# Optimization experiments

Measured on AMD Instinct MI355X. Metric: run time of the kernel, lower is better.

## Reference

```python
import math
import jax, jax.numpy as jnp
import numpy as np

B, T, DIN, DH, E, TOPK = 2048, 512, 32, 96, 6, 2


def setup_inputs() -> dict:
    key = jax.random.key(0)
    ks = jax.random.split(key, 20)
    x = jax.random.normal(ks[0], (B, T, DIN), jnp.float32)
    lengths = jax.random.randint(ks[1], (B,), 1, T + 1)
    mask = (jnp.arange(T)[None, :] < lengths[:, None])

    def U(k, shape, fan):
        s = 1.0 / math.sqrt(fan)
        return jax.random.uniform(k, shape, jnp.float32, -s, s)

    # PyTorch LSTM init: U(-1/sqrt(DH), 1/sqrt(DH)); gate order i,f,g,o
    Wih = U(ks[2], (4 * DH, DIN), DH)
    Whh = U(ks[3], (4 * DH, DH), DH)
    bih = U(ks[4], (4 * DH,), DH)
    bhh = U(ks[5], (4 * DH,), DH)
    Wq = U(ks[6], (DH, DH), DH); bq = U(ks[7], (DH,), DH)
    Wk = U(ks[8], (DH, DH), DH); bk = U(ks[9], (DH,), DH)
    Wv = U(ks[10], (DH, DH), DH); bv = U(ks[11], (DH,), DH)
    Wg = U(ks[12], (E, 2 * DH), 2 * DH); bg = U(ks[13], (E,), 2 * DH)
    We1 = U(ks[14], (E, DH, 2 * DH), 2 * DH); be1 = U(ks[15], (E, DH), 2 * DH)
    We2 = U(ks[16], (E, DH), DH); be2 = U(ks[17], (E,), DH)
    return dict(x=x, lengths=lengths, mask=mask, Wih=Wih, Whh=Whh, bih=bih, bhh=bhh,
                Wq=Wq, bq=bq, Wk=Wk, bk=bk, Wv=Wv, bv=bv, Wg=Wg, bg=bg,
                We1=We1, be1=be1, We2=We2, be2=be2)


def _lstm(x, mask, Wih, Whh, bih, bhh):
    # packed-sequence semantics: carry frozen past each sample's length,
    # padded output positions zeroed (like pad_packed_sequence).
    xg = x @ Wih.T + bih  # [B,T,4*DH] precomputed input projection
    dh = Whh.shape[1]

    def step(carry, inp):
        h, c = carry
        xg_t, m_t = inp
        g = xg_t + h @ Whh.T + bhh
        i, f, gg, o = jnp.split(g, 4, axis=-1)
        c_new = jax.nn.sigmoid(f) * c + jax.nn.sigmoid(i) * jnp.tanh(gg)
        h_new = jax.nn.sigmoid(o) * jnp.tanh(c_new)
        m = m_t[:, None]
        h = jnp.where(m, h_new, h)
        c = jnp.where(m, c_new, c)
        return (h, c), jnp.where(m, h_new, 0.0)

    init = (jnp.zeros((x.shape[0], dh), x.dtype), jnp.zeros((x.shape[0], dh), x.dtype))
    (hT, _), H = jax.lax.scan(step, init, (jnp.swapaxes(xg, 0, 1), mask.T))
    return jnp.swapaxes(H, 0, 1), hT  # H:[B,T,DH], hT:[B,DH]


def reference(x, lengths, mask, Wih, Whh, bih, bhh, Wq, bq, Wk, bk, Wv, bv,
              Wg, bg, We1, be1, We2, be2):
    H, hT = _lstm(x, mask, Wih, Whh, bih, bhh)
    Q = hT @ Wq.T + bq                      # [B,DH]
    K = H @ Wk.T + bk                       # [B,T,DH]
    V = H @ Wv.T + bv                       # [B,T,DH]
    logits = jnp.einsum('bd,btd->bt', Q, K) / math.sqrt(K.shape[-1])
    logits = jnp.where(mask, logits, -1e9)
    alpha = jax.nn.softmax(logits, axis=1)  # [B,T]
    ctx = jnp.einsum('bt,btd->bd', alpha, V)
    feats = jnp.concatenate([ctx, hT], axis=-1)  # [B,2*DH]
    gate_logits = feats @ Wg.T + bg              # [B,E]
    topv, topi = jax.lax.top_k(gate_logits, TOPK)
    pi = jax.nn.softmax(topv, axis=-1)           # [B,TOPK]
    # all-expert dense compute (E tiny), then gather selected -> same math as
    # the per-expert masked scatter loop in the torch module (dropout off).
    h1 = jax.nn.relu(jnp.einsum('bf,ehf->beh', feats, We1) + be1[None])  # [B,E,DH]
    outs = jnp.einsum('beh,eh->be', h1, We2) + be2[None]                  # [B,E]
    sel = jnp.take_along_axis(outs, topi, axis=1)                         # [B,TOPK]
    yhat = jnp.sum(pi * sel, axis=-1, keepdims=True)                      # [B,1]
    return yhat, alpha, gate_logits
```

## Files before the change

### kernel.cpp

```cpp
#include <hip/hip_runtime.h>
#include <hip/hip_bf16.h>

#define B_ 2048
#define T_ 512
#define DIN_ 32
#define DH_ 96
#define NG_ 384
#define E_ 6

#define BPB 8
#define HP 104
#define GS 10

typedef __attribute__((ext_vector_type(8))) _Float16 f16x8;
typedef __attribute__((ext_vector_type(4))) float f32x4;

#if defined(__has_builtin)
# if __has_builtin(__builtin_amdgcn_exp2f)
#  define EXP2F(x) __builtin_amdgcn_exp2f(x)
# endif
# if __has_builtin(__builtin_amdgcn_rcpf)
#  define RCPF(x) __builtin_amdgcn_rcpf(x)
# endif
#endif
#ifndef EXP2F
# define EXP2F(x) exp2f(x)
#endif
#ifndef RCPF
# define RCPF(x) (1.0f/(x))
#endif

__device__ __forceinline__ float sigf(float x) {
    return RCPF(1.0f + EXP2F(x * -1.44269504f));
}
__device__ __forceinline__ float tanhf_(float x) {
    return 1.0f - 2.0f * RCPF(1.0f + EXP2F(x * 2.88539008f));
}

__device__ __forceinline__ f16x8 cvt8(float4 a, float4 b) {
    f16x8 r;
    r[0] = (_Float16)a.x; r[1] = (_Float16)a.y; r[2] = (_Float16)a.z; r[3] = (_Float16)a.w;
    r[4] = (_Float16)b.x; r[5] = (_Float16)b.y; r[6] = (_Float16)b.z; r[7] = (_Float16)b.w;
    return r;
}
__device__ __forceinline__ f16x8 cvt8p(const float* p) {
    return cvt8(*(const float4*)p, *(const float4*)(p + 4));
}

__device__ __forceinline__ void lds_barrier() {
    asm volatile("s_waitcnt lgkmcnt(0)\n\ts_barrier" ::: "memory");
}

__global__ __launch_bounds__(512) void sort_kernel(
    const int* __restrict__ lengths, int* __restrict__ perm) {
    __shared__ int sbins[512];
    __shared__ int soffs[512];
    const int tid = threadIdx.x;
    sbins[tid] = 0;
    __syncthreads();
    for (int b = tid; b < B_; b += 512) atomicAdd(&sbins[lengths[b] - 1], 1);
    __syncthreads();
    soffs[tid] = sbins[tid];
    __syncthreads();
    for (int d = 1; d < 512; d <<= 1) {
        int v = (tid >= d) ? soffs[tid - d] : 0;
        __syncthreads();
        soffs[tid] += v;
        __syncthreads();
    }
    int excl = soffs[tid] - sbins[tid];
    __syncthreads();
    soffs[tid] = excl;
    __syncthreads();
    for (int b = tid; b < B_; b += 512) {
        const int pos = atomicAdd(&soffs[lengths[b] - 1], 1);
        perm[pos] = b;
    }
}

__global__ __launch_bounds__(768, 1) void lstm_kernel(
    const float* __restrict__ x, const int* __restrict__ lengths,
    const int* __restrict__ perm,
    const float* __restrict__ Wih, const float* __restrict__ Whh,
    const float* __restrict__ bih, const float* __restrict__ bhh,
    _Float16* __restrict__ Hout, float* __restrict__ hT)
{
    __shared__ float sgate[NG_ * GS];
    __shared__ _Float16 sh[2][8 * HP];
    __shared__ int sgb[BPB], slen[BPB];

    const int tid  = threadIdx.x;
    const int bb   = blockIdx.x * BPB;
    const int wave = tid >> 6;
    const int lane = tid & 63;
    const int col  = lane & 15;
    const int quad = lane >> 4;

    if (tid < BPB) {
        const int g = perm[bb + tid];
        sgb[tid] = g;
        slen[tid] = lengths[g];
    }
    {
        _Float16* shf = &sh[0][0];
        for (int i = tid; i < 2 * 8 * HP; i += 768) shf[i] = (_Float16)0.f;
    }
    __syncthreads();

    int bmax = slen[0];
#pragma unroll
    for (int i = 1; i < BPB; ++i) bmax = max(bmax, slen[i]);

    int gc[2]; float bias[2];
    f16x8 wh[2][3], wi[2];
#pragma unroll
    for (int j = 0; j < 2; ++j) {
        const int tau = wave * 2 + j;
        const int g = tau / 6, u6 = tau % 6;
        const int gcj = g * DH_ + u6 * 16 + col;
        gc[j] = gcj;
#pragma unroll
        for (int kf = 0; kf < 3; ++kf)
            wh[j][kf] = cvt8p(Whh + gcj * DH_ + kf * 32 + quad * 8);
        wi[j] = cvt8p(Wih + gcj * DIN_ + quad * 8);
        bias[j] = bih[gcj] + bhh[gcj];
    }

    const int eu = tid >> 3;
    const int eb = tid & 7;
    float c1 = 0.f, hk1 = 0.f;
    const int len1 = slen[eb];

    const bool st_act = tid < 384;
    const int sb = tid / 48;
    const int su = (tid % 48) * 2;
    _Float16* Hst = Hout + ((long long)sgb[sb] * T_) * DH_ + su;

    const bool arow = col < 8;
    const float* xp = x + ((long long)sgb[col & 7] * T_) * DIN_ + quad * 8;
    float4 xc0 = make_float4(0.f, 0.f, 0.f, 0.f), xc1 = xc0;
    if (arow) { xc0 = *(const float4*)xp; xc1 = *(const float4*)(xp + 4); }

    for (int t = 0; t < bmax; ++t) {
        const int buf = t & 1;

        f16x8 h0 = 0, h1 = 0, h2 = 0;
        if (arow) {
            const _Float16* hrow = &sh[buf][col * HP];
            h0 = *(const f16x8*)(hrow + 0  + quad * 8);
            h1 = *(const f16x8*)(hrow + 32 + quad * 8);
            h2 = *(const f16x8*)(hrow + 64 + quad * 8);
        }

        const float* xpn = (t + 1 < T_) ? (xp + DIN_) : xp;
        float4 xn0 = make_float4(0.f, 0.f, 0.f, 0.f), xn1 = xn0;
        if (arow) { xn0 = *(const float4*)xpn; xn1 = *(const float4*)(xpn + 4); }

        f16x8 xa = cvt8(xc0, xc1);

#pragma unroll
        for (int j = 0; j < 2; ++j) {
            f32x4 a = {bias[j], bias[j], bias[j], bias[j]};
            a = __builtin_amdgcn_mfma_f32_16x16x32_f16(h0, wh[j][0], a, 0, 0, 0);
            a = __builtin_amdgcn_mfma_f32_16x16x32_f16(h1, wh[j][1], a, 0, 0, 0);
            a = __builtin_amdgcn_mfma_f32_16x16x32_f16(h2, wh[j][2], a, 0, 0, 0);
            a = __builtin_amdgcn_mfma_f32_16x16x32_f16(xa, wi[j],    a, 0, 0, 0);
            if (quad < 2) {
                float2* sp = (float2*)&sgate[gc[j] * GS + quad * 4];
                sp[0] = float2{a[0], a[1]};
                sp[1] = float2{a[2], a[3]};
            }
        }
        lds_barrier();

        if (t > 0 && st_act) {
            unsigned v = *(const unsigned*)&sh[buf][sb * HP + su];
            *(unsigned*)Hst = v;
            Hst += DH_;
        }

        {
            float iv = sgate[(0 * DH_ + eu) * GS + eb];
            float fv = sgate[(1 * DH_ + eu) * GS + eb];
            float gv = sgate[(2 * DH_ + eu) * GS + eb];
            float ov = sgate[(3 * DH_ + eu) * GS + eb];
            float cn = sigf(fv) * c1 + sigf(iv) * tanhf_(gv);
            float hn = sigf(ov) * tanhf_(cn);
            const bool m = t < len1;
            c1  = m ? cn : c1;
            hk1 = m ? hn : hk1;
            sh[buf ^ 1][eb * HP + eu] = (_Float16)hk1;
        }
        lds_barrier();

        xp = xpn; xc0 = xn0; xc1 = xn1;
    }

    if (st_act) {
        unsigned v = *(const unsigned*)&sh[bmax & 1][sb * HP + su];
        *(unsigned*)Hst = v;
    }

    hT[sgb[eb] * DH_ + eu] = hk1;
}

__global__ __launch_bounds__(256) void attn_moe_kernel(
    const _Float16* __restrict__ H, const float* __restrict__ hT,
    const int* __restrict__ lengths,
    const float* __restrict__ Wq, const float* __restrict__ bq,
    const float* __restrict__ Wk, const float* __restrict__ bk,
    const float* __restrict__ Wv, const float* __restrict__ bv,
    const float* __restrict__ Wg, const float* __restrict__ bg,
    const float* __restrict__ We1, const float* __restrict__ be1,
    const float* __restrict__ We2, const float* __restrict__ be2,
    float* __restrict__ yhat_out, float* __restrict__ alpha_out,
    float* __restrict__ gl_out)
{
    __shared__ float salpha[T_];
    __shared__ float shT[DH_];
    __shared__ float sQ[DH_];
    __shared__ float sqk[DH_];
    __shared__ float spart[DH_];
    __shared__ float sfeats[2 * DH_];
    __shared__ float sh1[2][DH_];
    __shared__ float sred[4], ssum[4];
    __shared__ float sgl[E_];
    __shared__ float spi[2];
    __shared__ float souts[2];
    __shared__ float sqb_s;
    __shared__ int stopi[2];

    const int b = blockIdx.x, tid = threadIdx.x;
    const int len = lengths[b];
    const float scale = 0.10206207262f;

    if (tid < DH_) shT[tid] = hT[b * DH_ + tid];
    __syncthreads();
    if (tid < DH_) {
        float acc = bq[tid];
        const float* wr = Wq + tid * DH_;
        for (int d = 0; d < DH_; d += 4) {
            float4 w4 = *(const float4*)(wr + d);
            acc += w4.x * shT[d] + w4.y * shT[d + 1] + w4.z * shT[d + 2] + w4.w * shT[d + 3];
        }
        sQ[tid] = acc;
    }
    __syncthreads();
    if (tid < DH_) {
        float acc = 0.f;
        for (int j = 0; j < DH_; ++j) acc += Wk[j * DH_ + tid] * sQ[j];
        sqk[tid] = acc * scale;
    }
    if (tid >= 192) {
        const int ln = tid - 192;
        float p = sQ[ln] * bk[ln];
        if (ln < DH_ - 64) p += sQ[ln + 64] * bk[ln + 64];
        for (int off = 32; off; off >>= 1) p += __shfl_xor(p, off);
        if (ln == 0) sqb_s = p * scale;
    }
    __syncthreads();
    const float qbv = sqb_s;

    float lg[2]; bool vd[2];
#pragma unroll
    for (int hh = 0; hh < 2; ++hh) {
        const int t = tid + hh * 256;
        vd[hh] = t < len;
        float l = qbv;
        if (vd[hh]) {
            const _Float16* hr = H + ((long long)b * T_ + t) * DH_;
#pragma unroll
            for (int u = 0; u < DH_; u += 8) {
                f16x8 hv = *(const f16x8*)(hr + u);
                float4 qa = *(const float4*)&sqk[u];
                float4 qc = *(const float4*)&sqk[u + 4];
                l += (float)hv[0] * qa.x + (float)hv[1] * qa.y
                   + (float)hv[2] * qa.z + (float)hv[3] * qa.w
                   + (float)hv[4] * qc.x + (float)hv[5] * qc.y
                   + (float)hv[6] * qc.z + (float)hv[7] * qc.w;
            }
        }
        lg[hh] = l;
    }

    float m = fmaxf(vd[0] ? lg[0] : -1e30f, vd[1] ? lg[1] : -1e30f);
    for (int off = 32; off; off >>= 1) m = fmaxf(m, __shfl_xor(m, off));
    if ((tid & 63) == 0) sred[tid >> 6] = m;
    __syncthreads();
    m = fmaxf(fmaxf(sred[0], sred[1]), fmaxf(sred[2], sred[3]));

    float e0 = vd[0] ? EXP2F((lg[0] - m) * 1.44269504f) : 0.f;
    float e1 = vd[1] ? EXP2F((lg[1] - m) * 1.44269504f) : 0.f;
    float s = e0 + e1;
    for (int off = 32; off; off >>= 1) s += __shfl_xor(s, off);
    if ((tid & 63) == 0) ssum[tid >> 6] = s;
    __syncthreads();
    s = (ssum[0] + ssum[1]) + (ssum[2] + ssum[3]);

    const float rinv = RCPF(s);
    const float a0 = e0 * rinv, a1 = e1 * rinv;
    salpha[tid] = a0;
    salpha[tid + 256] = a1;
    alpha_out[(long long)b * T_ + tid] = a0;
    alpha_out[(long long)b * T_ + tid + 256] = a1;
    __syncthreads();

    if (tid < 192) {
        const int ub = tid >> 4, tl = tid & 15;
        float acc[8] = {0.f, 0.f, 0.f, 0.f, 0.f, 0.f, 0.f, 0.f};
        const _Float16* hb = H + ((long long)b * T_) * DH_ + ub * 8;
#pragma unroll 4
        for (int k = 0; k < 32; ++k) {
            const int t = tl + (k << 4);
            if (t < len) {
                f16x8 hv = *(const f16x8*)(hb + t * DH_);
                const float a = salpha[t];
#pragma unroll
                for (int i = 0; i < 8; ++i) acc[i] += a * (float)hv[i];
            }
        }
#pragma unroll
        for (int i = 0; i < 8; ++i) {
            acc[i] += __shfl_xor(acc[i], 1);
            acc[i] += __shfl_xor(acc[i], 2);
            acc[i] += __shfl_xor(acc[i], 4);
            acc[i] += __shfl_xor(acc[i], 8);
        }
        if (tl == 0) {
#pragma unroll
            for (int i = 0; i < 8; ++i) spart[ub * 8 + i] = acc[i];
        }
    }
    __syncthreads();

    if (tid < DH_) {
        float acc = bv[tid];
        const float* wr = Wv + tid * DH_;
        for (int u = 0; u < DH_; u += 4) {
            float4 w4 = *(const float4*)(wr + u);
            acc += w4.x * spart[u] + w4.y * spart[u + 1] + w4.z * spart[u + 2] + w4.w * spart[u + 3];
        }
        sfeats[tid] = acc;
        sfeats[DH_ + tid] = shT[tid];
    }
    __syncthreads();

    if (tid < 192) {
        const int e6 = tid >> 5, cc = tid & 31;
        float p = 0.f;
        const float* wg = Wg + e6 * 2 * DH_;
#pragma unroll
        for (int j = 0; j < 6; ++j) p += wg[cc * 6 + j] * sfeats[cc * 6 + j];
        for (int off = 16; off; off >>= 1) p += __shfl_xor(p, off);
        if (cc == 0) {
            float g = p + bg[e6];
            sgl[e6] = g;
            gl_out[b * E_ + e6] = g;
        }
    }
    __syncthreads();

    if (tid == 0) {
        int i0 = 0; float v0 = sgl[0];
        for (int ee = 1; ee < E_; ++ee) if (sgl[ee] > v0) { v0 = sgl[ee]; i0 = ee; }
        int i1 = -1; float v1 = -1e30f;
        for (int ee = 0; ee < E_; ++ee) {
            if (ee == i0) continue;
            if (sgl[ee] > v1) { v1 = sgl[ee]; i1 = ee; }
        }
        float ex1 = EXP2F((v1 - v0) * 1.44269504f);
        float inv = RCPF(1.f + ex1);
        spi[0] = inv; spi[1] = ex1 * inv;
        stopi[0] = i0; stopi[1] = i1;
    }
    __syncthreads();

    if (tid < 192) {
        const int e2 = tid / DH_, u = tid - e2 * DH_;
        const int ex = stopi[e2];
        float acc = be1[ex * DH_ + u];
        const float* w = We1 + ((long long)ex * DH_ + u) * (2 * DH_);
        for (int f = 0; f < 2 * DH_; f += 4) {
            float4 w4 = *(const float4*)(w + f);
            acc += w4.x * sfeats[f] + w4.y * sfeats[f + 1] + w4.z * sfeats[f + 2] + w4.w * sfeats[f + 3];
        }
        sh1[e2][u] = fmaxf(acc, 0.f);
    }
    __syncthreads();

    if (tid < 128) {
        const int e2 = tid >> 6, ln = tid & 63;
        const int ex = stopi[e2];
        const float* w2 = We2 + ex * DH_;
        float p = sh1[e2][ln] * w2[ln];
        if (ln < DH_ - 64) p += sh1[e2][ln + 64] * w2[ln + 64];
        for (int off = 32; off; off >>= 1) p += __shfl_xor(p, off);
        if (ln == 0) souts[e2] = p + be2[ex];
    }
    __syncthreads();
    if (tid == 0)
        yhat_out[b] = spi[0] * souts[0] + spi[1] * souts[1];
}

extern "C" void kernel_launch(void* const* d_in, const int* in_sizes, int n_in,
                              void* d_out, int out_size, void* d_ws, size_t ws_size,
                              hipStream_t stream) {
    const float* x   = (const float*)d_in[0];
    const int* lengths = (const int*)d_in[1];
    const float* Wih = (const float*)d_in[3];
    const float* Whh = (const float*)d_in[4];
    const float* bih = (const float*)d_in[5];
    const float* bhh = (const float*)d_in[6];
    const float* Wq  = (const float*)d_in[7];
    const float* bq  = (const float*)d_in[8];
    const float* Wk  = (const float*)d_in[9];
    const float* bk  = (const float*)d_in[10];
    const float* Wv  = (const float*)d_in[11];
    const float* bv  = (const float*)d_in[12];
    const float* Wg  = (const float*)d_in[13];
    const float* bg  = (const float*)d_in[14];
    const float* We1 = (const float*)d_in[15];
    const float* be1 = (const float*)d_in[16];
    const float* We2 = (const float*)d_in[17];
    const float* be2 = (const float*)d_in[18];

    float* yhat  = (float*)d_out;
    float* alpha = yhat + B_;
    float* gl    = alpha + (size_t)B_ * T_;

    char* ws = (char*)d_ws;
    _Float16* Hws = (_Float16*)ws;
    float* hTws = (float*)(ws + (size_t)B_ * T_ * DH_ * 2);
    int* perm   = (int*)(hTws + (size_t)B_ * DH_);

    sort_kernel<<<dim3(1), dim3(512), 0, stream>>>(lengths, perm);

    lstm_kernel<<<dim3(B_ / BPB), dim3(768), 0, stream>>>(
        x, lengths, perm, Wih, Whh, bih, bhh, Hws, hTws);
    attn_moe_kernel<<<dim3(B_), dim3(256), 0, stream>>>(
        Hws, hTws, lengths, Wq, bq, Wk, bk, Wv, bv, Wg, bg,
        We1, be1, We2, be2, yhat, alpha, gl);
}
```

Before: 697.9 us.

## Interleave two 8-sample LSTM groups per block to overlap MFMA with gate math

Each LSTM block now processes 16 sorted samples as two groups of 8. Their steps are software-pipelined so that one group's gate MFMAs run alongside the other group's elementwise cell update and H store, with a double-buffered gate array. This halves the block count and is meant to hide the serial matmul→activation latency of the recurrence. In exchange each step does more work between barriers, and bmax is now taken over 16 samples, which adds padding steps.

```diff
diff --git a/kernel.cpp b/kernel.cpp
--- a/kernel.cpp
+++ b/kernel.cpp
@@ -8,9 +8,9 @@
 #define NG_ 384
 #define E_ 6
 
-#define BPB 8
+#define BPB 16
 #define HP 104
-#define GS 10
+#define GS 12
 
 typedef __attribute__((ext_vector_type(8))) _Float16 f16x8;
 typedef __attribute__((ext_vector_type(4))) float f32x4;
@@ -85,8 +85,8 @@
     const float* __restrict__ bih, const float* __restrict__ bhh,
     _Float16* __restrict__ Hout, float* __restrict__ hT)
 {
-    __shared__ float sgate[NG_ * GS];
-    __shared__ _Float16 sh[2][8 * HP];
+    __shared__ float sgate[2][NG_ * GS];
+    __shared__ _Float16 sh[BPB * HP];
     __shared__ int sgb[BPB], slen[BPB];
 
     const int tid  = threadIdx.x;
@@ -101,10 +101,7 @@
         sgb[tid] = g;
         slen[tid] = lengths[g];
     }
-    {
-        _Float16* shf = &sh[0][0];
-        for (int i = tid; i < 2 * 8 * HP; i += 768) shf[i] = (_Float16)0.f;
-    }
+    for (int i = tid; i < BPB * HP; i += 768) sh[i] = (_Float16)0.f;
     __syncthreads();
 
     int bmax = slen[0];
@@ -128,35 +125,40 @@
 
     const int eu = tid >> 3;
     const int eb = tid & 7;
-    float c1 = 0.f, hk1 = 0.f;
-    const int len1 = slen[eb];
-
-    const bool st_act = tid < 384;
-    const int sb = tid / 48;
-    const int su = (tid % 48) * 2;
-    _Float16* Hst = Hout + ((long long)sgb[sb] * T_) * DH_ + su;
+    float cA = 0.f, hkA = 0.f, cB = 0.f, hkB = 0.f;
+    const int lenA = slen[eb];
+    const int lenB = slen[8 + eb];
+
+    const bool stA = tid < 384;
+    const int sbA = (tid / 48) & 7;
+    const int suA = (tid % 48) * 2;
+    const int sbB = ((tid - 384) / 48) & 7;
+    const int suB = ((tid - 384) % 48) * 2;
+    _Float16* HstA = Hout + ((long long)sgb[sbA] * T_) * DH_ + suA;
+    _Float16* HstB = Hout + ((long long)sgb[8 + sbB] * T_) * DH_ + suB;
 
     const bool arow = col < 8;
-    const float* xp = x + ((long long)sgb[col & 7] * T_) * DIN_ + quad * 8;
-    float4 xc0 = make_float4(0.f, 0.f, 0.f, 0.f), xc1 = xc0;
-    if (arow) { xc0 = *(const float4*)xp; xc1 = *(const float4*)(xp + 4); }
+    const float* xpA = x + ((long long)sgb[col & 7] * T_) * DIN_ + quad * 8;
+    const float* xpB = x + ((long long)sgb[8 + (col & 7)] * T_) * DIN_ + quad * 8;
+    float4 z4 = make_float4(0.f, 0.f, 0.f, 0.f);
+    float4 xA0 = z4, xA1 = z4, xB0 = z4, xB1 = z4;
+    if (arow) {
+        xA0 = *(const float4*)xpA; xA1 = *(const float4*)(xpA + 4);
+        xB0 = *(const float4*)xpB; xB1 = *(const float4*)(xpB + 4);
+    }
 
     for (int t = 0; t < bmax; ++t) {
-        const int buf = t & 1;
-
         f16x8 h0 = 0, h1 = 0, h2 = 0;
         if (arow) {
-            const _Float16* hrow = &sh[buf][col * HP];
-            h0 = *(const f16x8*)(hrow + 0  + quad * 8);
-            h1 = *(const f16x8*)(hrow + 32 + quad * 8);
-            h2 = *(const f16x8*)(hrow + 64 + quad * 8);
-        }
-
-        const float* xpn = (t + 1 < T_) ? (xp + DIN_) : xp;
-        float4 xn0 = make_float4(0.f, 0.f, 0.f, 0.f), xn1 = xn0;
-        if (arow) { xn0 = *(const float4*)xpn; xn1 = *(const float4*)(xpn + 4); }
-
-        f16x8 xa = cvt8(xc0, xc1);
+            const _Float16* hr = &sh[col * HP];
+            h0 = *(const f16x8*)(hr + 0  + quad * 8);
+            h1 = *(const f16x8*)(hr + 32 + quad * 8);
+            h2 = *(const f16x8*)(hr + 64 + quad * 8);
+        }
+        const float* xpAn = (t + 1 < T_) ? (xpA + DIN_) : xpA;
+        float4 xAn0 = z4, xAn1 = z4;
+        if (arow) { xAn0 = *(const float4*)xpAn; xAn1 = *(const float4*)(xpAn + 4); }
+        f16x8 xa = cvt8(xA0, xA1);
 
 #pragma unroll
         for (int j = 0; j < 2; ++j) {
@@ -165,43 +167,99 @@
             a = __builtin_amdgcn_mfma_f32_16x16x32_f16(h1, wh[j][1], a, 0, 0, 0);
             a = __builtin_amdgcn_mfma_f32_16x16x32_f16(h2, wh[j][2], a, 0, 0, 0);
             a = __builtin_amdgcn_mfma_f32_16x16x32_f16(xa, wi[j],    a, 0, 0, 0);
-            if (quad < 2) {
-                float2* sp = (float2*)&sgate[gc[j] * GS + quad * 4];
-                sp[0] = float2{a[0], a[1]};
-                sp[1] = float2{a[2], a[3]};
-            }
+            if (quad < 2)
+                *(f32x4*)&sgate[0][gc[j] * GS + quad * 4] = a;
+        }
+
+        if (t > 0) {
+            float iv = sgate[1][(0 * DH_ + eu) * GS + eb];
+            float fv = sgate[1][(1 * DH_ + eu) * GS + eb];
+            float gv = sgate[1][(2 * DH_ + eu) * GS + eb];
+            float ov = sgate[1][(3 * DH_ + eu) * GS + eb];
+            float cn = sigf(fv) * cB + sigf(iv) * tanhf_(gv);
+            float hn = sigf(ov) * tanhf_(cn);
+            const bool m = (t - 1) < lenB;
+            cB  = m ? cn : cB;
+            hkB = m ? hn : hkB;
+            sh[(8 + eb) * HP + eu] = (_Float16)hkB;
+        }
+        if (t > 0 && stA) {
+            unsigned v = *(const unsigned*)&sh[sbA * HP + suA];
+            *(unsigned*)HstA = v;
+            HstA += DH_;
         }
         lds_barrier();
 
-        if (t > 0 && st_act) {
-            unsigned v = *(const unsigned*)&sh[buf][sb * HP + su];
-            *(unsigned*)Hst = v;
-            Hst += DH_;
+        f16x8 g0 = 0, g1 = 0, g2 = 0;
+        if (arow) {
+            const _Float16* hr = &sh[(8 + col) * HP];
+            g0 = *(const f16x8*)(hr + 0  + quad * 8);
+            g1 = *(const f16x8*)(hr + 32 + quad * 8);
+            g2 = *(const f16x8*)(hr + 64 + quad * 8);
+        }
+        const float* xpBn = (t + 1 < T_) ? (xpB + DIN_) : xpB;
+        float4 xBn0 = z4, xBn1 = z4;
+        if (arow) { xBn0 = *(const float4*)xpBn; xBn1 = *(const float4*)(xpBn + 4); }
+        f16x8 xb = cvt8(xB0, xB1);
+
+#pragma unroll
+        for (int j = 0; j < 2; ++j) {
+            f32x4 a = {bias[j], bias[j], bias[j], bias[j]};
+            a = __builtin_amdgcn_mfma_f32_16x16x32_f16(g0, wh[j][0], a, 0, 0, 0);
+            a = __builtin_amdgcn_mfma_f32_16x16x32_f16(g1, wh[j][1], a, 0, 0, 0);
+            a = __builtin_amdgcn_mfma_f32_16x16x32_f16(g2, wh[j][2], a, 0, 0, 0);
+            a = __builtin_amdgcn_mfma_f32_16x16x32_f16(xb, wi[j],    a, 0, 0, 0);
+            if (quad < 2)
+                *(f32x4*)&sgate[1][gc[j] * GS + quad * 4] = a;
         }
 
         {
-            float iv = sgate[(0 * DH_ + eu) * GS + eb];
-            float fv = sgate[(1 * DH_ + eu) * GS + eb];
-            float gv = sgate[(2 * DH_ + eu) * GS + eb];
-            float ov = sgate[(3 * DH_ + eu) * GS + eb];
-            float cn = sigf(fv) * c1 + sigf(iv) * tanhf_(gv);
+            float iv = sgate[0][(0 * DH_ + eu) * GS + eb];
+            float fv = sgate[0][(1 * DH_ + eu) * GS + eb];
+            float gv = sgate[0][(2 * DH_ + eu) * GS + eb];
+            float ov = sgate[0][(3 * DH_ + eu) * GS + eb];
+            float cn = sigf(fv) * cA + sigf(iv) * tanhf_(gv);
             float hn = sigf(ov) * tanhf_(cn);
-            const bool m = t < len1;
-            c1  = m ? cn : c1;
-            hk1 = m ? hn : hk1;
-            sh[buf ^ 1][eb * HP + eu] = (_Float16)hk1;
+            const bool m = t < lenA;
+            cA  = m ? cn : cA;
+            hkA = m ? hn : hkA;
+            sh[eb * HP + eu] = (_Float16)hkA;
+        }
+        if (t > 0 && !stA) {
+            unsigned v = *(const unsigned*)&sh[(8 + sbB) * HP + suB];
+            *(unsigned*)HstB = v;
+            HstB += DH_;
         }
         lds_barrier();
 
-        xp = xpn; xc0 = xn0; xc1 = xn1;
-    }
-
-    if (st_act) {
-        unsigned v = *(const unsigned*)&sh[bmax & 1][sb * HP + su];
-        *(unsigned*)Hst = v;
-    }
-
-    hT[sgb[eb] * DH_ + eu] = hk1;
+        xpA = xpAn; xA0 = xAn0; xA1 = xAn1;
+        xpB = xpBn; xB0 = xBn0; xB1 = xBn1;
+    }
+
+    {
+        float iv = sgate[1][(0 * DH_ + eu) * GS + eb];
+        float fv = sgate[1][(1 * DH_ + eu) * GS + eb];
+        float gv = sgate[1][(2 * DH_ + eu) * GS + eb];
+        float ov = sgate[1][(3 * DH_ + eu) * GS + eb];
+        float cn = sigf(fv) * cB + sigf(iv) * tanhf_(gv);
+        float hn = sigf(ov) * tanhf_(cn);
+        const bool m = (bmax - 1) < lenB;
+        cB  = m ? cn : cB;
+        hkB = m ? hn : hkB;
+        sh[(8 + eb) * HP + eu] = (_Float16)hkB;
+    }
+    if (stA) {
+        unsigned v = *(const unsigned*)&sh[sbA * HP + suA];
+        *(unsigned*)HstA = v;
+    }
+    lds_barrier();
+    if (!stA) {
+        unsigned v = *(const unsigned*)&sh[(8 + sbB) * HP + suB];
+        *(unsigned*)HstB = v;
+    }
+
+    hT[sgb[eb] * DH_ + eu] = hkA;
+    hT[sgb[8 + eb] * DH_ + eu] = hkB;
 }
 
 __global__ __launch_bounds__(256) void attn_moe_kernel(
```

Measured after the change: 1.229 ms. 76.1% more time.

## Fuse attention and MoE head into the LSTM kernel epilogue

Applied to the files above, without the earlier changes.

Merges the separate attention/MoE kernel into the end of the LSTM kernel, so each 8-sample block computes its own Q, logits, softmax, context, gating and expert MLP right after the recurrence. This removes a kernel launch and the hT round trip through global memory. H is re-read while it may still sit in cache. The tail now runs on only 256 blocks of 768 threads with one block per CU, where the old separate kernel had 2048 blocks, so the attention phase may get less parallelism. It also adds about 35KB of extra shared memory.

```diff
diff --git a/kernel.cpp b/kernel.cpp
--- a/kernel.cpp
+++ b/kernel.cpp
@@ -78,16 +78,36 @@
     }
 }
 
-__global__ __launch_bounds__(768, 1) void lstm_kernel(
+__global__ __launch_bounds__(768, 1) void lstm_attn_kernel(
     const float* __restrict__ x, const int* __restrict__ lengths,
     const int* __restrict__ perm,
     const float* __restrict__ Wih, const float* __restrict__ Whh,
     const float* __restrict__ bih, const float* __restrict__ bhh,
-    _Float16* __restrict__ Hout, float* __restrict__ hT)
+    const float* __restrict__ Wq, const float* __restrict__ bq,
+    const float* __restrict__ Wk, const float* __restrict__ bk,
+    const float* __restrict__ Wv, const float* __restrict__ bv,
+    const float* __restrict__ Wg, const float* __restrict__ bg,
+    const float* __restrict__ We1, const float* __restrict__ be1,
+    const float* __restrict__ We2, const float* __restrict__ be2,
+    _Float16* __restrict__ Hout,
+    float* __restrict__ yhat_out, float* __restrict__ alpha_out,
+    float* __restrict__ gl_out)
 {
     __shared__ float sgate[NG_ * GS];
     __shared__ _Float16 sh[2][8 * HP];
     __shared__ int sgb[BPB], slen[BPB];
+    __shared__ float slog[BPB][T_];
+    __shared__ float shT8[BPB][DH_];
+    __shared__ float sQ8[BPB][DH_];
+    __shared__ float sqk8[BPB][DH_];
+    __shared__ float scraw[BPB][DH_];
+    __shared__ float sfeats[BPB][2 * DH_];
+    __shared__ float sh1_[BPB][2][DH_];
+    __shared__ float sqb[BPB];
+    __shared__ float sgl[BPB][E_];
+    __shared__ float spi2[BPB][2];
+    __shared__ float souts[BPB][2];
+    __shared__ int stopi2[BPB][2];
 
     const int tid  = threadIdx.x;
     const int bb   = blockIdx.x * BPB;
@@ -201,120 +221,100 @@
         *(unsigned*)Hst = v;
     }
 
-    hT[sgb[eb] * DH_ + eu] = hk1;
-}
-
-__global__ __launch_bounds__(256) void attn_moe_kernel(
-    const _Float16* __restrict__ H, const float* __restrict__ hT,
-    const int* __restrict__ lengths,
-    const float* __restrict__ Wq, const float* __restrict__ bq,
-    const float* __restrict__ Wk, const float* __restrict__ bk,
-    const float* __restrict__ Wv, const float* __restrict__ bv,
-    const float* __restrict__ Wg, const float* __restrict__ bg,
-    const float* __restrict__ We1, const float* __restrict__ be1,
-    const float* __restrict__ We2, const float* __restrict__ be2,
-    float* __restrict__ yhat_out, float* __restrict__ alpha_out,
-    float* __restrict__ gl_out)
-{
-    __shared__ float salpha[T_];
-    __shared__ float shT[DH_];
-    __shared__ float sQ[DH_];
-    __shared__ float sqk[DH_];
-    __shared__ float spart[DH_];
-    __shared__ float sfeats[2 * DH_];
-    __shared__ float sh1[2][DH_];
-    __shared__ float sred[4], ssum[4];
-    __shared__ float sgl[E_];
-    __shared__ float spi[2];
-    __shared__ float souts[2];
-    __shared__ float sqb_s;
-    __shared__ int stopi[2];
-
-    const int b = blockIdx.x, tid = threadIdx.x;
-    const int len = lengths[b];
+    shT8[eb][eu] = hk1;
+    __threadfence_block();
+    __syncthreads();
+
+    const int abi = tid / 96;
+    const int au  = tid - abi * 96;
+    const int ag  = sgb[abi];
+    const int alen = slen[abi];
     const float scale = 0.10206207262f;
 
-    if (tid < DH_) shT[tid] = hT[b * DH_ + tid];
-    __syncthreads();
-    if (tid < DH_) {
-        float acc = bq[tid];
-        const float* wr = Wq + tid * DH_;
+    {
+        float acc = bq[au];
+        const float* wr = Wq + au * DH_;
+        const float* ht = &shT8[abi][0];
         for (int d = 0; d < DH_; d += 4) {
             float4 w4 = *(const float4*)(wr + d);
-            acc += w4.x * shT[d] + w4.y * shT[d + 1] + w4.z * shT[d + 2] + w4.w * shT[d + 3];
-        }
-        sQ[tid] = acc;
-    }
-    __syncthreads();
-    if (tid < DH_) {
+            acc += w4.x * ht[d] + w4.y * ht[d + 1] + w4.z * ht[d + 2] + w4.w * ht[d + 3];
+        }
+        sQ8[abi][au] = acc;
+    }
+    __syncthreads();
+
+    {
         float acc = 0.f;
-        for (int j = 0; j < DH_; ++j) acc += Wk[j * DH_ + tid] * sQ[j];
-        sqk[tid] = acc * scale;
-    }
-    if (tid >= 192) {
-        const int ln = tid - 192;
-        float p = sQ[ln] * bk[ln];
-        if (ln < DH_ - 64) p += sQ[ln + 64] * bk[ln + 64];
+        const float* qv = &sQ8[abi][0];
+        for (int j = 0; j < DH_; ++j) acc += Wk[j * DH_ + au] * qv[j];
+        sqk8[abi][au] = acc * scale;
+    }
+    if (wave < 8) {
+        float p = sQ8[wave][lane] * bk[lane];
+        if (lane < 32) p += sQ8[wave][64 + lane] * bk[64 + lane];
         for (int off = 32; off; off >>= 1) p += __shfl_xor(p, off);
-        if (ln == 0) sqb_s = p * scale;
-    }
-    __syncthreads();
-    const float qbv = sqb_s;
-
-    float lg[2]; bool vd[2];
-#pragma unroll
-    for (int hh = 0; hh < 2; ++hh) {
-        const int t = tid + hh * 256;
-        vd[hh] = t < len;
-        float l = qbv;
-        if (vd[hh]) {
-            const _Float16* hr = H + ((long long)b * T_ + t) * DH_;
-#pragma unroll
-            for (int u = 0; u < DH_; u += 8) {
-                f16x8 hv = *(const f16x8*)(hr + u);
-                float4 qa = *(const float4*)&sqk[u];
-                float4 qc = *(const float4*)&sqk[u + 4];
-                l += (float)hv[0] * qa.x + (float)hv[1] * qa.y
-                   + (float)hv[2] * qa.z + (float)hv[3] * qa.w
-                   + (float)hv[4] * qc.x + (float)hv[5] * qc.y
-                   + (float)hv[6] * qc.z + (float)hv[7] * qc.w;
+        if (lane == 0) sqb[wave] = p * scale;
+    }
+    __syncthreads();
+
+    for (int k = 0; k < 6; ++k) {
+        const int r = tid + k * 768;
+        if (r < BPB * T_) {
+            const int bi2 = r >> 9, t = r & (T_ - 1);
+            float l = -1e30f;
+            if (t < slen[bi2]) {
+                const _Float16* hr = Hout + ((long long)sgb[bi2] * T_ + t) * DH_;
+                const float* qk = &sqk8[bi2][0];
+                float acc = sqb[bi2];
+#pragma unroll
+                for (int u = 0; u < DH_; u += 8) {
+                    f16x8 hv = *(const f16x8*)(hr + u);
+                    float4 qa = *(const float4*)(qk + u);
+                    float4 qc = *(const float4*)(qk + u + 4);
+                    acc += (float)hv[0] * qa.x + (float)hv[1] * qa.y
+                         + (float)hv[2] * qa.z + (float)hv[3] * qa.w
+                         + (float)hv[4] * qc.x + (float)hv[5] * qc.y
+                         + (float)hv[6] * qc.z + (float)hv[7] * qc.w;
+                }
+                l = acc;
             }
-        }
-        lg[hh] = l;
-    }
-
-    float m = fmaxf(vd[0] ? lg[0] : -1e30f, vd[1] ? lg[1] : -1e30f);
-    for (int off = 32; off; off >>= 1) m = fmaxf(m, __shfl_xor(m, off));
-    if ((tid & 63) == 0) sred[tid >> 6] = m;
-    __syncthreads();
-    m = fmaxf(fmaxf(sred[0], sred[1]), fmaxf(sred[2], sred[3]));
-
-    float e0 = vd[0] ? EXP2F((lg[0] - m) * 1.44269504f) : 0.f;
-    float e1 = vd[1] ? EXP2F((lg[1] - m) * 1.44269504f) : 0.f;
-    float s = e0 + e1;
-    for (int off = 32; off; off >>= 1) s += __shfl_xor(s, off);
-    if ((tid & 63) == 0) ssum[tid >> 6] = s;
-    __syncthreads();
-    s = (ssum[0] + ssum[1]) + (ssum[2] + ssum[3]);
-
-    const float rinv = RCPF(s);
-    const float a0 = e0 * rinv, a1 = e1 * rinv;
-    salpha[tid] = a0;
-    salpha[tid + 256] = a1;
-    alpha_out[(long long)b * T_ + tid] = a0;
-    alpha_out[(long long)b * T_ + tid + 256] = a1;
-    __syncthreads();
-
-    if (tid < 192) {
-        const int ub = tid >> 4, tl = tid & 15;
+            slog[0][r] = l;
+        }
+    }
+    __syncthreads();
+
+    if (wave < 8) {
+        float lv[8];
+#pragma unroll
+        for (int j = 0; j < 8; ++j) lv[j] = slog[wave][lane + 64 * j];
+        float m = lv[0];
+#pragma unroll
+        for (int j = 1; j < 8; ++j) m = fmaxf(m, lv[j]);
+        for (int off = 32; off; off >>= 1) m = fmaxf(m, __shfl_xor(m, off));
+        float ev[8]; float s = 0.f;
+#pragma unroll
+        for (int j = 0; j < 8; ++j) { ev[j] = EXP2F((lv[j] - m) * 1.44269504f); s += ev[j]; }
+        for (int off = 32; off; off >>= 1) s += __shfl_xor(s, off);
+        const float rinv = RCPF(s);
+        float* aout = alpha_out + (long long)sgb[wave] * T_;
+#pragma unroll
+        for (int j = 0; j < 8; ++j) {
+            const float a = ev[j] * rinv;
+            slog[wave][lane + 64 * j] = a;
+            aout[lane + 64 * j] = a;
+        }
+    }
+    __syncthreads();
+
+    {
+        const int ub = au >> 3, tl = au & 7;
         float acc[8] = {0.f, 0.f, 0.f, 0.f, 0.f, 0.f, 0.f, 0.f};
-        const _Float16* hb = H + ((long long)b * T_) * DH_ + ub * 8;
-#pragma unroll 4
-        for (int k = 0; k < 32; ++k) {
-            const int t = tl + (k << 4);
-            if (t < len) {
+        const _Float16* hb = Hout + ((long long)ag * T_) * DH_ + ub * 8;
+        for (int k = 0; k < 64; ++k) {
+            const int t = tl + (k << 3);
+            if (t < alen) {
                 f16x8 hv = *(const f16x8*)(hb + t * DH_);
-                const float a = salpha[t];
+                const float a = slog[abi][t];
 #pragma unroll
                 for (int i = 0; i < 8; ++i) acc[i] += a * (float)hv[i];
             }
@@ -324,82 +324,86 @@
             acc[i] += __shfl_xor(acc[i], 1);
             acc[i] += __shfl_xor(acc[i], 2);
             acc[i] += __shfl_xor(acc[i], 4);
-            acc[i] += __shfl_xor(acc[i], 8);
         }
         if (tl == 0) {
 #pragma unroll
-            for (int i = 0; i < 8; ++i) spart[ub * 8 + i] = acc[i];
-        }
-    }
-    __syncthreads();
-
-    if (tid < DH_) {
-        float acc = bv[tid];
-        const float* wr = Wv + tid * DH_;
-        for (int u = 0; u < DH_; u += 4) {
-            float4 w4 = *(const float4*)(wr + u);
-            acc += w4.x * spart[u] + w4.y * spart[u + 1] + w4.z * spart[u + 2] + w4.w * spart[u + 3];
-        }
-        sfeats[tid] = acc;
-        sfeats[DH_ + tid] = shT[tid];
-    }
-    __syncthreads();
-
-    if (tid < 192) {
-        const int e6 = tid >> 5, cc = tid & 31;
+            for (int i = 0; i < 8; ++i) scraw[abi][ub * 8 + i] = acc[i];
+        }
+    }
+    __syncthreads();
+
+    {
+        float acc = bv[au];
+        const float* wr = Wv + au * DH_;
+        const float* cr = &scraw[abi][0];
+        for (int u2 = 0; u2 < DH_; u2 += 4) {
+            float4 w4 = *(const float4*)(wr + u2);
+            acc += w4.x * cr[u2] + w4.y * cr[u2 + 1] + w4.z * cr[u2 + 2] + w4.w * cr[u2 + 3];
+        }
+        sfeats[abi][au] = acc;
+        sfeats[abi][DH_ + au] = shT8[abi][au];
+    }
+    __syncthreads();
+
+    {
+        const int ge = au >> 4, gcc = au & 15;
         float p = 0.f;
-        const float* wg = Wg + e6 * 2 * DH_;
-#pragma unroll
-        for (int j = 0; j < 6; ++j) p += wg[cc * 6 + j] * sfeats[cc * 6 + j];
-        for (int off = 16; off; off >>= 1) p += __shfl_xor(p, off);
-        if (cc == 0) {
-            float g = p + bg[e6];
-            sgl[e6] = g;
-            gl_out[b * E_ + e6] = g;
-        }
-    }
-    __syncthreads();
-
-    if (tid == 0) {
-        int i0 = 0; float v0 = sgl[0];
-        for (int ee = 1; ee < E_; ++ee) if (sgl[ee] > v0) { v0 = sgl[ee]; i0 = ee; }
+        const float* wg = Wg + ge * 2 * DH_ + gcc * 12;
+        const float* ft = &sfeats[abi][gcc * 12];
+#pragma unroll
+        for (int j = 0; j < 12; ++j) p += wg[j] * ft[j];
+        p += __shfl_xor(p, 1); p += __shfl_xor(p, 2);
+        p += __shfl_xor(p, 4); p += __shfl_xor(p, 8);
+        if (gcc == 0) {
+            const float g2 = p + bg[ge];
+            sgl[abi][ge] = g2;
+            gl_out[ag * E_ + ge] = g2;
+        }
+    }
+    __syncthreads();
+
+    if (tid < BPB) {
+        int i0 = 0; float v0 = sgl[tid][0];
+        for (int ee = 1; ee < E_; ++ee) if (sgl[tid][ee] > v0) { v0 = sgl[tid][ee]; i0 = ee; }
         int i1 = -1; float v1 = -1e30f;
         for (int ee = 0; ee < E_; ++ee) {
             if (ee == i0) continue;
-            if (sgl[ee] > v1) { v1 = sgl[ee]; i1 = ee; }
-        }
-        float ex1 = EXP2F((v1 - v0) * 1.44269504f);
-        float inv = RCPF(1.f + ex1);
-        spi[0] = inv; spi[1] = ex1 * inv;
-        stopi[0] = i0; stopi[1] = i1;
-    }
-    __syncthreads();
-
-    if (tid < 192) {
-        const int e2 = tid / DH_, u = tid - e2 * DH_;
-        const int ex = stopi[e2];
-        float acc = be1[ex * DH_ + u];
-        const float* w = We1 + ((long long)ex * DH_ + u) * (2 * DH_);
+            if (sgl[tid][ee] > v1) { v1 = sgl[tid][ee]; i1 = ee; }
+        }
+        const float ex1 = EXP2F((v1 - v0) * 1.44269504f);
+        const float inv = RCPF(1.f + ex1);
+        spi2[tid][0] = inv; spi2[tid][1] = ex1 * inv;
+        stopi2[tid][0] = i0; stopi2[tid][1] = i1;
+    }
+    __syncthreads();
+
+#pragma unroll
+    for (int e2 = 0; e2 < 2; ++e2) {
+        const int ex = stopi2[abi][e2];
+        float acc = be1[ex * DH_ + au];
+        const float* w = We1 + ((long long)ex * DH_ + au) * (2 * DH_);
+        const float* ft = &sfeats[abi][0];
         for (int f = 0; f < 2 * DH_; f += 4) {
             float4 w4 = *(const float4*)(w + f);
-            acc += w4.x * sfeats[f] + w4.y * sfeats[f + 1] + w4.z * sfeats[f + 2] + w4.w * sfeats[f + 3];
-        }
-        sh1[e2][u] = fmaxf(acc, 0.f);
-    }
-    __syncthreads();
-
-    if (tid < 128) {
-        const int e2 = tid >> 6, ln = tid & 63;
-        const int ex = stopi[e2];
+            acc += w4.x * ft[f] + w4.y * ft[f + 1] + w4.z * ft[f + 2] + w4.w * ft[f + 3];
+        }
+        sh1_[abi][e2][au] = fmaxf(acc, 0.f);
+    }
+    __syncthreads();
+
+    if (wave < 8) {
+        const int e2 = lane >> 5, lu = lane & 31;
+        const int ex = stopi2[wave][e2];
         const float* w2 = We2 + ex * DH_;
-        float p = sh1[e2][ln] * w2[ln];
-        if (ln < DH_ - 64) p += sh1[e2][ln + 64] * w2[ln + 64];
-        for (int off = 32; off; off >>= 1) p += __shfl_xor(p, off);
-        if (ln == 0) souts[e2] = p + be2[ex];
-    }
-    __syncthreads();
-    if (tid == 0)
-        yhat_out[b] = spi[0] * souts[0] + spi[1] * souts[1];
+        const float* h1p = &sh1_[wave][e2][0];
+        float p = h1p[lu] * w2[lu] + h1p[lu + 32] * w2[lu + 32] + h1p[lu + 64] * w2[lu + 64];
+        p += __shfl_xor(p, 1); p += __shfl_xor(p, 2); p += __shfl_xor(p, 4);
+        p += __shfl_xor(p, 8); p += __shfl_xor(p, 16);
+        if (lu == 0) souts[wave][e2] = p + be2[ex];
+    }
+    __syncthreads();
+    if (tid < BPB)
+        yhat_out[sgb[tid]] = spi2[tid][0] * souts[tid][0] + spi2[tid][1] * souts[tid][1];
 }
 
 extern "C" void kernel_launch(void* const* d_in, const int* in_sizes, int n_in,
@@ -430,14 +434,12 @@
 
     char* ws = (char*)d_ws;
     _Float16* Hws = (_Float16*)ws;
-    float* hTws = (float*)(ws + (size_t)B_ * T_ * DH_ * 2);
-    int* perm   = (int*)(hTws + (size_t)B_ * DH_);
+    int* perm   = (int*)(ws + (size_t)B_ * T_ * DH_ * 2);
 
     sort_kernel<<<dim3(1), dim3(512), 0, stream>>>(lengths, perm);
 
-    lstm_kernel<<<dim3(B_ / BPB), dim3(768), 0, stream>>>(
-        x, lengths, perm, Wih, Whh, bih, bhh, Hws, hTws);
-    attn_moe_kernel<<<dim3(B_), dim3(256), 0, stream>>>(
-        Hws, hTws, lengths, Wq, bq, Wk, bk, Wv, bv, Wg, bg,
-        We1, be1, We2, be2, yhat, alpha, gl);
-}
+    lstm_attn_kernel<<<dim3(B_ / BPB), dim3(768), 0, stream>>>(
+        x, lengths, perm, Wih, Whh, bih, bhh,
+        Wq, bq, Wk, bk, Wv, bv, Wg, bg, We1, be1, We2, be2,
+        Hws, yhat, alpha, gl);
+}
```

Result: slower. 718.6 us (+3.0%).
